# Kernel optimization log

Measured on AMD Instinct MI355X. Metric: run time of the kernel, lower is better.

Reference implementation:

```python
import jax, jax.numpy as jnp
import numpy as np

B = 64
A_DIM, T_DIM, V_DIM = 512, 1024, 512
H = 96
O1, O2, O3 = 6, 1, 3
HP1 = H + 1  # 97


def setup_inputs() -> dict:
    key = jax.random.key(0)
    ks = jax.random.split(key, 20)
    s = 0.02
    inp = {
        "audios": jax.random.normal(ks[0], (B, A_DIM), jnp.float32),
        "texts": jax.random.normal(ks[1], (B, T_DIM), jnp.float32),
        "videos": jax.random.normal(ks[2], (B, V_DIM), jnp.float32),
        # MLP encoders: Linear(in, hidden) + ReLU (dropout is identity at eval)
        "Wa": jax.random.normal(ks[3], (A_DIM, H), jnp.float32) * s,
        "ba": jnp.zeros((H,), jnp.float32),
        "Wt": jax.random.normal(ks[4], (T_DIM, H), jnp.float32) * s,
        "bt": jnp.zeros((H,), jnp.float32),
        "Wv": jax.random.normal(ks[5], (V_DIM, H), jnp.float32) * s,
        "bv": jnp.zeros((H,), jnp.float32),
        # post-fusion MLP
        "W1": jax.random.normal(ks[6], (HP1 * HP1 * HP1, H), jnp.float32) * s,
        "b1": jnp.zeros((H,), jnp.float32),
        "W2": jax.random.normal(ks[7], (H, H), jnp.float32) * s,
        "b2": jnp.zeros((H,), jnp.float32),
        # output heads
        "Wo1": jax.random.normal(ks[8], (H, O1), jnp.float32) * s,
        "bo1": jnp.zeros((O1,), jnp.float32),
        "Wo2": jax.random.normal(ks[9], (H, O2), jnp.float32) * s,
        "bo2": jnp.zeros((O2,), jnp.float32),
        "Wo3": jax.random.normal(ks[10], (H, O3), jnp.float32) * s,
        "bo3": jnp.zeros((O3,), jnp.float32),
    }
    return inp


def reference(audios, texts, videos, Wa, ba, Wt, bt, Wv, bv,
              W1, b1, W2, b2, Wo1, bo1, Wo2, bo2, Wo3, bo3):
    # encoders (eval mode: dropout = identity)
    ah = jax.nn.relu(audios @ Wa + ba)   # [B, H]
    th = jax.nn.relu(texts @ Wt + bt)    # [B, H]
    vh = jax.nn.relu(videos @ Wv + bv)   # [B, H]

    one = jnp.ones((ah.shape[0], 1), ah.dtype)
    a1 = jnp.concatenate([one, ah], axis=1)  # [B, H+1]
    v1 = jnp.concatenate([one, vh], axis=1)  # [B, H+1]
    t1 = jnp.concatenate([one, th], axis=1)  # [B, H+1]

    # trilinear outer product: bmm(a1[:, :, None], v1[:, None, :]) -> [B, A, V]
    # then bmm with t1 -> [B, A*V, T]; flatten order is (a, v, t)
    fusion = jnp.einsum('ba,bv,bt->bavt', a1, v1, t1).reshape(a1.shape[0], -1)

    y1 = jax.nn.relu(fusion @ W1 + b1)
    features = jax.nn.relu(y1 @ W2 + b2)

    emos_out = features @ Wo1 + bo1
    vals_out = features @ Wo2 + bo2
    sents_out = features @ Wo3 + bo3
    interloss = jnp.zeros((), jnp.float32)
    return (features, emos_out, vals_out, sents_out, interloss)
```

## Files before the change

kernel.cpp:

```cpp
#include <hip/hip_runtime.h>


typedef unsigned int u32;
typedef short frag8s __attribute__((ext_vector_type(8)));
typedef float f32x4 __attribute__((ext_vector_type(4)));

constexpr int G3     = 589;
constexpr int NRUN   = 9409;
constexpr int NRUNP  = 9412;
constexpr int NGROUP = 2353;
constexpr int RBLK   = 776;

constexpr int WS_A1T  = 0;
constexpr int WS_V1T  = WS_A1T + 98 * 64;
constexpr int WS_T1T  = WS_V1T + 98 * 64;
constexpr int WS_T1PK = WS_T1T + 98 * 64;
constexpr int WS_S    = WS_T1PK + 64 * 64;
constexpr int WS_WAT  = WS_S + NRUNP * 64;
constexpr int WS_WTT  = WS_WAT + 96 * 512;
constexpr int WS_WVT  = WS_WTT + 96 * 1024;
constexpr int WS_PART = WS_WVT + 96 * 512;
constexpr int WS_PART2= WS_PART + G3 * 6144;

__device__ __forceinline__ u32 bfrne(float x) {
    u32 u = __float_as_uint(x);
    return (u + 0x7FFFu + ((u >> 16) & 1u)) >> 16;
}
__device__ __forceinline__ float bflo(u32 p) { return __uint_as_float(p << 16); }
__device__ __forceinline__ float bfhi(u32 p) { return __uint_as_float(p & 0xFFFF0000u); }

__device__ __forceinline__ void async_cp16(float* lds, const float* g) {
    __builtin_amdgcn_global_load_lds((const __attribute__((address_space(1))) u32*)g,
                                     (__attribute__((address_space(3))) u32*)lds, 16, 0, 0);
}
__device__ __forceinline__ void async_cp4(float* lds, const float* g) {
    __builtin_amdgcn_global_load_lds((const __attribute__((address_space(1))) u32*)g,
                                     (__attribute__((address_space(3))) u32*)lds, 4, 0, 0);
}

__global__ void k0_transpose(const float* __restrict__ Wa, const float* __restrict__ Wt,
                             const float* __restrict__ Wv, float* __restrict__ ws) {
    int idx = blockIdx.x * 256 + threadIdx.x;
    if (idx < 49152) {
        int h = idx / 512, k = idx % 512;
        ws[WS_WAT + h * 512 + k] = Wa[k * 96 + h];
    } else if (idx < 147456) {
        int i = idx - 49152; int h = i / 1024, k = i % 1024;
        ws[WS_WTT + h * 1024 + k] = Wt[k * 96 + h];
    } else if (idx < 196608) {
        int i = idx - 147456; int h = i / 512, k = i % 512;
        ws[WS_WVT + h * 512 + k] = Wv[k * 96 + h];
    }
}

__global__ __launch_bounds__(256) void k1_enc(const float* __restrict__ audios,
                                              const float* __restrict__ texts,
                                              const float* __restrict__ videos,
                                              const float* __restrict__ ba,
                                              const float* __restrict__ bt,
                                              const float* __restrict__ bv,
                                              float* __restrict__ ws) {
    int wg = blockIdx.x, tid = threadIdx.x;
    int lane = tid & 63, wv = tid >> 6;
    if (wg == 288) {
        if (tid < 64) ws[WS_T1T + 97 * 64 + tid] = 0.0f;
        return;
    }
    int e = wg / 96, h = wg % 96;
    const float* in; const float* wt; float bias; int K; int outbase;
    if (e == 0)      { in = audios; wt = ws + WS_WAT + h * 512;  bias = ba[h]; K = 512;  outbase = WS_A1T; }
    else if (e == 1) { in = texts;  wt = ws + WS_WTT + h * 1024; bias = bt[h]; K = 1024; outbase = WS_T1T; }
    else             { in = videos; wt = ws + WS_WVT + h * 512;  bias = bv[h]; K = 512;  outbase = WS_V1T; }
    int nsweep = K >> 8;
    float4 wreg[4];
    for (int s = 0; s < nsweep; s++) wreg[s] = ((const float4*)wt)[s * 64 + lane];
    for (int pass = 0; pass < 16; pass++) {
        int b = pass * 4 + wv;
        float acc = 0.f;
        for (int s = 0; s < nsweep; s++) {
            float4 iv = ((const float4*)(in + b * K))[s * 64 + lane];
            acc += iv.x * wreg[s].x + iv.y * wreg[s].y + iv.z * wreg[s].z + iv.w * wreg[s].w;
        }
        for (int off = 32; off; off >>= 1) acc += __shfl_down(acc, off, 64);
        if (lane == 0) {
            float v = acc + bias;
            ws[outbase + (h + 1) * 64 + b] = v > 0.f ? v : 0.f;
        }
    }
    if (h == 0 && tid < 64) ws[outbase + tid] = 1.0f;
}

__global__ __launch_bounds__(256) void k2_s(float* __restrict__ ws) {
    int wg = blockIdx.x, tid = threadIdx.x;
    u32* t1pk = (u32*)ws + WS_T1PK;
    if (wg == 589) {
        for (int i = tid; i < 4096; i += 256) {
            int b = i >> 6, p = i & 63;
            u32 v = 0;
            if (p < 49) {
                float e0 = ws[WS_T1T + (2 * p) * 64 + b];
                float e1 = ws[WS_T1T + (2 * p + 1) * 64 + b];
                v = bfrne(e0) | (bfrne(e1) << 16);
            }
            t1pk[i] = v;
        }
        return;
    }
    for (int ii = 0; ii < 4; ii++) {
        int idx = wg * 1024 + ii * 256 + tid;
        if (idx >= NRUNP * 64) break;
        int run = idx >> 6, b = idx & 6 * 10 + 3;
        b = idx & 63;
        float s = 0.f;
        if (run < NRUN) {
            int i = run / 97, j = run % 97;
            s = ws[WS_A1T + i * 64 + b] * ws[WS_V1T + j * 64 + b];
        }
        ws[WS_S + idx] = s;
    }
}

__global__ __launch_bounds__(256) void k3_main(const float* __restrict__ W1,
                                               float* __restrict__ ws) {
    __shared__ float wtile[2][4 * RBLK];
    __shared__ u32   tpk[64 * 65];
    __shared__ float sl[2][4 * 64];

    int tid = threadIdx.x, lane = tid & 63, wv = tid >> 6;
    int id = blockIdx.x;
    const u32* t1pk_g = (const u32*)ws + WS_T1PK;
    const float* s_g = ws + WS_S;

    for (int i = tid; i < 2 * 4 * RBLK / 4; i += 256)
        ((float4*)wtile)[i] = make_float4(0.f, 0.f, 0.f, 0.f);
    for (int i = tid; i < 4096; i += 256) {
        int b = i >> 6, p = i & 63;
        tpk[b * 65 + p] = t1pk_g[i];
    }

    int glist[4]; int gcount = 0;
    for (int i2 = 0; i2 < 4; i2++) { int g = id + i2 * G3; if (g < NGROUP) glist[gcount++] = g; }

    f32x4 acc[6];
    for (int nt = 0; nt < 6; nt++) acc[nt] = f32x4{0.f, 0.f, 0.f, 0.f};

    auto stage_w = [&](int g, int koff, int buf) {
        int run = g * 4 + wv; if (run > 9408) run = 9408;
        if (koff < 96) {
            const float* gsrc = W1 + (size_t)(run * 97 + koff) * 96;
            float* ldst = &wtile[buf][wv * RBLK];
            for (int c = 0; c < 3; c++)
                async_cp16(ldst + c * 256, gsrc + c * 256 + lane * 4);
        } else {
            if (lane < 24)
                async_cp16(&wtile[buf][wv * RBLK], W1 + (size_t)(run * 97 + 96) * 96 + lane * 4);
        }
    };
    auto stage_s = [&](int g, int sb) {
        if (wv == 0) {
            for (int q2 = 0; q2 < 4; q2++) {
                int run = g * 4 + q2;
                async_cp4(&sl[sb][q2 * 64], s_g + run * 64 + lane);
            }
        }
    };

    stage_s(glist[0], 0);
    stage_w(glist[0], 0, 0);
    __syncthreads();

    int pw = 0, sb = 0;
    int b = (wv << 4) + (lane & 15);
    int q = lane >> 4;

    for (int gi = 0; gi < gcount; gi++) {
        int g = glist[gi];
        for (int step = 0; step < 13; step++) {
            int koff = step * 8;
            if (step < 12) stage_w(g, koff + 8, pw ^ 1);
            else if (gi + 1 < gcount) { stage_w(glist[gi + 1], 0, pw ^ 1); stage_s(glist[gi + 1], sb ^ 1); }

            float s = sl[sb][q * 64 + b];
            int pb = b * 65 + (koff >> 1);
            u32 ap[4];
#pragma unroll
            for (int r = 0; r < 4; r++) {
                u32 tp = tpk[pb + r];
                float fe = s * bflo(tp), fo = s * bfhi(tp);
                ap[r] = bfrne(fe) | (bfrne(fo) << 16);
            }
            union { u32 u[4]; frag8s f; } afr;
            afr.u[0] = ap[0]; afr.u[1] = ap[1]; afr.u[2] = ap[2]; afr.u[3] = ap[3];

            const float* wt0 = &wtile[pw][q * RBLK + (lane & 15)];
#pragma unroll
            for (int nt = 0; nt < 6; nt++) {
                union { u32 u[4]; frag8s f; } bfr;
#pragma unroll
                for (int r = 0; r < 4; r++) {
                    u32 w0 = __float_as_uint(wt0[(2 * r) * 96 + nt * 16]);
                    u32 w1 = __float_as_uint(wt0[(2 * r + 1) * 96 + nt * 16]);
                    bfr.u[r] = (w0 >> 16) | (w1 & 0xFFFF0000u);
                }
                acc[nt] = __builtin_amdgcn_mfma_f32_16x16x32_bf16(afr.f, bfr.f, acc[nt], 0, 0, 0);
            }
            __syncthreads();
            pw ^= 1;
        }
        sb ^= 1;
    }

    float* part = ws + WS_PART + (size_t)id * 6144;
#pragma unroll
    for (int nt = 0; nt < 6; nt++) {
#pragma unroll
        for (int r = 0; r < 4; r++) {
            int row = (wv << 4) + ((lane >> 4) << 2) + r;
            int col = nt * 16 + (lane & 15);
            part[row * 96 + col] = acc[nt][r];
        }
    }
}

__global__ __launch_bounds__(256) void k4a_reduce(float* __restrict__ ws) {
    int bid = blockIdx.x;
    int oc = bid % 24, wc = bid / 24;
    int o = oc * 256 + threadIdx.x;
    int w0 = wc * 74, w1 = w0 + 74; if (w1 > G3) w1 = G3;
    const float* part = ws + WS_PART + o;
    float a0 = 0.f, a1 = 0.f;
    int w = w0;
    for (; w + 2 <= w1; w += 2) {
        a0 += part[(size_t)w * 6144];
        a1 += part[(size_t)(w + 1) * 6144];
    }
    for (; w < w1; w++) a0 += part[(size_t)w * 6144];
    ws[WS_PART2 + (size_t)wc * 6144 + o] = a0 + a1;
}

__global__ __launch_bounds__(256) void k5_final(const float* __restrict__ b1,
                                                const float* __restrict__ W2, const float* __restrict__ b2,
                                                const float* __restrict__ Wo1, const float* __restrict__ bo1,
                                                const float* __restrict__ Wo2, const float* __restrict__ bo2,
                                                const float* __restrict__ Wo3, const float* __restrict__ bo3,
                                                const float* __restrict__ ws, float* __restrict__ out) {
    __shared__ float yl[8 * 96];
    __shared__ float w2l[96 * 97];
    __shared__ float fl[8 * 96];
    int tid = threadIdx.x;
    int row0 = blockIdx.x * 8;
    for (int i = tid; i < 768; i += 256) {
        int go = row0 * 96 + i;
        float acc = b1[i % 96];
#pragma unroll
        for (int w = 0; w < 8; w++) acc += ws[WS_PART2 + (size_t)w * 6144 + go];
        yl[i] = acc > 0.f ? acc : 0.f;
    }
    for (int i = tid; i < 9216; i += 256) { int k = i / 96, h = i % 96; w2l[k * 97 + h] = W2[i]; }
    __syncthreads();
    for (int i = tid; i < 768; i += 256) {
        int bb = i / 96, h = i % 96;
        float acc = b2[h];
#pragma unroll 8
        for (int k = 0; k < 96; k++) acc += yl[bb * 96 + k] * w2l[k * 97 + h];
        float f = acc > 0.f ? acc : 0.f;
        fl[i] = f; out[(row0 + bb) * 96 + h] = f;
    }
    __syncthreads();
    if (tid < 80) {
        if (tid < 48) {
            int lr = tid / 6, j = tid % 6;
            float acc = bo1[j];
            for (int k = 0; k < 96; k++) acc += fl[lr * 96 + k] * Wo1[k * 6 + j];
            out[6144 + (row0 + lr) * 6 + j] = acc;
        } else if (tid < 56) {
            int lr = tid - 48;
            float acc = bo2[0];
            for (int k = 0; k < 96; k++) acc += fl[lr * 96 + k] * Wo2[k];
            out[6528 + row0 + lr] = acc;
        } else {
            int t2 = tid - 56; int lr = t2 / 3, j = t2 % 3;
            float acc = bo3[j];
            for (int k = 0; k < 96; k++) acc += fl[lr * 96 + k] * Wo3[k * 3 + j];
            out[6592 + (row0 + lr) * 3 + j] = acc;
        }
    }
    if (blockIdx.x == 0 && tid == 0) out[6784] = 0.0f;
}

extern "C" void kernel_launch(void* const* d_in, const int* in_sizes, int n_in,
                              void* d_out, int out_size, void* d_ws, size_t ws_size,
                              hipStream_t stream) {
    (void)in_sizes; (void)n_in; (void)out_size; (void)ws_size;
    const float* audios = (const float*)d_in[0];
    const float* texts  = (const float*)d_in[1];
    const float* videos = (const float*)d_in[2];
    const float* Wa  = (const float*)d_in[3];
    const float* ba  = (const float*)d_in[4];
    const float* Wt  = (const float*)d_in[5];
    const float* bt  = (const float*)d_in[6];
    const float* Wv  = (const float*)d_in[7];
    const float* bv  = (const float*)d_in[8];
    const float* W1  = (const float*)d_in[9];
    const float* b1  = (const float*)d_in[10];
    const float* W2  = (const float*)d_in[11];
    const float* b2  = (const float*)d_in[12];
    const float* Wo1 = (const float*)d_in[13];
    const float* bo1 = (const float*)d_in[14];
    const float* Wo2 = (const float*)d_in[15];
    const float* bo2 = (const float*)d_in[16];
    const float* Wo3 = (const float*)d_in[17];
    const float* bo3 = (const float*)d_in[18];
    float* ws = (float*)d_ws;
    float* outp = (float*)d_out;

    k0_transpose<<<768, 256, 0, stream>>>(Wa, Wt, Wv, ws);
    k1_enc<<<289, 256, 0, stream>>>(audios, texts, videos, ba, bt, bv, ws);
    k2_s<<<590, 256, 0, stream>>>(ws);
    k3_main<<<G3, 256, 0, stream>>>(W1, ws);
    k4a_reduce<<<192, 256, 0, stream>>>(ws);
    k5_final<<<8, 256, 0, stream>>>(b1, W2, b2, Wo1, bo1, Wo2, bo2, Wo3, bo3, ws, outp);
}
```

Before: 583.8 us.

## Fuse prep kernels into main GEMM, deepen W1 pipeline, reduce via atomics

Result: faster. 565.5 us (-3.1%).

```diff
diff --git a/kernel.cpp b/kernel.cpp
--- a/kernel.cpp
+++ b/kernel.cpp
@@ -5,22 +5,16 @@
 typedef short frag8s __attribute__((ext_vector_type(8)));
 typedef float f32x4 __attribute__((ext_vector_type(4)));
 
-constexpr int G3     = 589;
 constexpr int NRUN   = 9409;
-constexpr int NRUNP  = 9412;
 constexpr int NGROUP = 2353;
 constexpr int RBLK   = 776;
-
-constexpr int WS_A1T  = 0;
-constexpr int WS_V1T  = WS_A1T + 98 * 64;
-constexpr int WS_T1T  = WS_V1T + 98 * 64;
-constexpr int WS_T1PK = WS_T1T + 98 * 64;
-constexpr int WS_S    = WS_T1PK + 64 * 64;
-constexpr int WS_WAT  = WS_S + NRUNP * 64;
-constexpr int WS_WTT  = WS_WAT + 96 * 512;
-constexpr int WS_WVT  = WS_WTT + 96 * 1024;
-constexpr int WS_PART = WS_WVT + 96 * 512;
-constexpr int WS_PART2= WS_PART + G3 * 6144;
+constexpr int NW1    = 912673 * 96;
+constexpr int G3     = 512;
+
+constexpr int WS_A1T   = 0;
+constexpr int WS_V1T   = WS_A1T + 98 * 64;
+constexpr int WS_T1T   = WS_V1T + 98 * 64;
+constexpr int WS_Y1SUM = WS_T1T + 98 * 64;
 
 __device__ __forceinline__ u32 bfrne(float x) {
     u32 u = __float_as_uint(x);
@@ -33,47 +27,33 @@
     __builtin_amdgcn_global_load_lds((const __attribute__((address_space(1))) u32*)g,
                                      (__attribute__((address_space(3))) u32*)lds, 16, 0, 0);
 }
-__device__ __forceinline__ void async_cp4(float* lds, const float* g) {
-    __builtin_amdgcn_global_load_lds((const __attribute__((address_space(1))) u32*)g,
-                                     (__attribute__((address_space(3))) u32*)lds, 4, 0, 0);
-}
-
-__global__ void k0_transpose(const float* __restrict__ Wa, const float* __restrict__ Wt,
-                             const float* __restrict__ Wv, float* __restrict__ ws) {
-    int idx = blockIdx.x * 256 + threadIdx.x;
-    if (idx < 49152) {
-        int h = idx / 512, k = idx % 512;
-        ws[WS_WAT + h * 512 + k] = Wa[k * 96 + h];
-    } else if (idx < 147456) {
-        int i = idx - 49152; int h = i / 1024, k = i % 1024;
-        ws[WS_WTT + h * 1024 + k] = Wt[k * 96 + h];
-    } else if (idx < 196608) {
-        int i = idx - 147456; int h = i / 512, k = i % 512;
-        ws[WS_WVT + h * 512 + k] = Wv[k * 96 + h];
-    }
-}
 
 __global__ __launch_bounds__(256) void k1_enc(const float* __restrict__ audios,
                                               const float* __restrict__ texts,
                                               const float* __restrict__ videos,
-                                              const float* __restrict__ ba,
-                                              const float* __restrict__ bt,
-                                              const float* __restrict__ bv,
+                                              const float* __restrict__ Wa, const float* __restrict__ ba,
+                                              const float* __restrict__ Wt, const float* __restrict__ bt,
+                                              const float* __restrict__ Wv, const float* __restrict__ bv,
                                               float* __restrict__ ws) {
     int wg = blockIdx.x, tid = threadIdx.x;
     int lane = tid & 63, wv = tid >> 6;
     if (wg == 288) {
         if (tid < 64) ws[WS_T1T + 97 * 64 + tid] = 0.0f;
+        for (int i = tid; i < 6144; i += 256) ws[WS_Y1SUM + i] = 0.0f;
         return;
     }
     int e = wg / 96, h = wg % 96;
-    const float* in; const float* wt; float bias; int K; int outbase;
-    if (e == 0)      { in = audios; wt = ws + WS_WAT + h * 512;  bias = ba[h]; K = 512;  outbase = WS_A1T; }
-    else if (e == 1) { in = texts;  wt = ws + WS_WTT + h * 1024; bias = bt[h]; K = 1024; outbase = WS_T1T; }
-    else             { in = videos; wt = ws + WS_WVT + h * 512;  bias = bv[h]; K = 512;  outbase = WS_V1T; }
+    const float* in; const float* W; float bias; int K; int outbase;
+    if (e == 0)      { in = audios; W = Wa; bias = ba[h]; K = 512;  outbase = WS_A1T; }
+    else if (e == 1) { in = texts;  W = Wt; bias = bt[h]; K = 1024; outbase = WS_T1T; }
+    else             { in = videos; W = Wv; bias = bv[h]; K = 512;  outbase = WS_V1T; }
     int nsweep = K >> 8;
     float4 wreg[4];
-    for (int s = 0; s < nsweep; s++) wreg[s] = ((const float4*)wt)[s * 64 + lane];
+    for (int s = 0; s < nsweep; s++) {
+        int k0i = s * 256 + lane * 4;
+        wreg[s] = make_float4(W[(k0i + 0) * 96 + h], W[(k0i + 1) * 96 + h],
+                              W[(k0i + 2) * 96 + h], W[(k0i + 3) * 96 + h]);
+    }
     for (int pass = 0; pass < 16; pass++) {
         int b = pass * 4 + wv;
         float acc = 0.f;
@@ -90,152 +70,117 @@
     if (h == 0 && tid < 64) ws[outbase + tid] = 1.0f;
 }
 
-__global__ __launch_bounds__(256) void k2_s(float* __restrict__ ws) {
-    int wg = blockIdx.x, tid = threadIdx.x;
-    u32* t1pk = (u32*)ws + WS_T1PK;
-    if (wg == 589) {
-        for (int i = tid; i < 4096; i += 256) {
-            int b = i >> 6, p = i & 63;
-            u32 v = 0;
-            if (p < 49) {
-                float e0 = ws[WS_T1T + (2 * p) * 64 + b];
-                float e1 = ws[WS_T1T + (2 * p + 1) * 64 + b];
-                v = bfrne(e0) | (bfrne(e1) << 16);
-            }
-            t1pk[i] = v;
-        }
-        return;
-    }
-    for (int ii = 0; ii < 4; ii++) {
-        int idx = wg * 1024 + ii * 256 + tid;
-        if (idx >= NRUNP * 64) break;
-        int run = idx >> 6, b = idx & 6 * 10 + 3;
-        b = idx & 63;
-        float s = 0.f;
-        if (run < NRUN) {
-            int i = run / 97, j = run % 97;
-            s = ws[WS_A1T + i * 64 + b] * ws[WS_V1T + j * 64 + b];
-        }
-        ws[WS_S + idx] = s;
-    }
-}
-
 __global__ __launch_bounds__(256) void k3_main(const float* __restrict__ W1,
                                                float* __restrict__ ws) {
-    __shared__ float wtile[2][4 * RBLK];
+    __shared__ float wtile[4][4 * RBLK];
     __shared__ u32   tpk[64 * 65];
-    __shared__ float sl[2][4 * 64];
+    __shared__ float sl[5][256];
 
     int tid = threadIdx.x, lane = tid & 63, wv = tid >> 6;
     int id = blockIdx.x;
-    const u32* t1pk_g = (const u32*)ws + WS_T1PK;
-    const float* s_g = ws + WS_S;
-
-    for (int i = tid; i < 2 * 4 * RBLK / 4; i += 256)
-        ((float4*)wtile)[i] = make_float4(0.f, 0.f, 0.f, 0.f);
+    int g0, gcount;
+    if (id < 305) { g0 = id * 5;                 gcount = 5; }
+    else          { g0 = 1525 + (id - 305) * 4;  gcount = 4; }
+    const int L = gcount * 13;
+
     for (int i = tid; i < 4096; i += 256) {
-        int b = i >> 6, p = i & 63;
-        tpk[b * 65 + p] = t1pk_g[i];
-    }
-
-    int glist[4]; int gcount = 0;
-    for (int i2 = 0; i2 < 4; i2++) { int g = id + i2 * G3; if (g < NGROUP) glist[gcount++] = g; }
+        int b_ = i >> 6, p = i & 63;
+        u32 v = 0;
+        if (p < 49) {
+            float e0 = ws[WS_T1T + (2 * p) * 64 + b_];
+            float e1 = ws[WS_T1T + (2 * p + 1) * 64 + b_];
+            v = bfrne(e0) | (bfrne(e1) << 16);
+        }
+        tpk[b_ * 65 + p] = v;
+    }
+    {
+        int q2 = tid >> 6, b_ = tid & 63;
+#pragma unroll
+        for (int g2 = 0; g2 < 5; g2++) {
+            float s = 0.f;
+            int run = (g0 + g2) * 4 + q2;
+            if (g2 < gcount && run < NRUN) {
+                int i = run / 97, j = run % 97;
+                s = ws[WS_A1T + i * 64 + b_] * ws[WS_V1T + j * 64 + b_];
+            }
+            sl[g2][tid] = s;
+        }
+    }
+
+    auto stage = [&](int g, int t, int buf) {
+        int idx0 = (g * 4 + wv) * (97 * 96) + t * (8 * 96) + lane * 4;
+        float* ldst = &wtile[buf][wv * RBLK];
+#pragma unroll
+        for (int c = 0; c < 3; c++) {
+            int idx = idx0 + c * 256;
+            idx = idx < NW1 - 4 ? idx : NW1 - 4;
+            async_cp16(ldst + c * 256, W1 + idx);
+        }
+    };
+    int cs_g = g0, cs_t = 0;
+    auto stage_next = [&](int buf) {
+        stage(cs_g, cs_t, buf);
+        if (++cs_t == 13) { cs_t = 0; ++cs_g; }
+    };
+
+    stage_next(0); stage_next(1); stage_next(2);
+    asm volatile("s_waitcnt vmcnt(6) lgkmcnt(0)" ::: "memory");
+    __builtin_amdgcn_s_barrier();
 
     f32x4 acc[6];
+#pragma unroll
     for (int nt = 0; nt < 6; nt++) acc[nt] = f32x4{0.f, 0.f, 0.f, 0.f};
 
-    auto stage_w = [&](int g, int koff, int buf) {
-        int run = g * 4 + wv; if (run > 9408) run = 9408;
-        if (koff < 96) {
-            const float* gsrc = W1 + (size_t)(run * 97 + koff) * 96;
-            float* ldst = &wtile[buf][wv * RBLK];
-            for (int c = 0; c < 3; c++)
-                async_cp16(ldst + c * 256, gsrc + c * 256 + lane * 4);
-        } else {
-            if (lane < 24)
-                async_cp16(&wtile[buf][wv * RBLK], W1 + (size_t)(run * 97 + 96) * 96 + lane * 4);
-        }
-    };
-    auto stage_s = [&](int g, int sb) {
-        if (wv == 0) {
-            for (int q2 = 0; q2 < 4; q2++) {
-                int run = g * 4 + q2;
-                async_cp4(&sl[sb][q2 * 64], s_g + run * 64 + lane);
-            }
-        }
-    };
-
-    stage_s(glist[0], 0);
-    stage_w(glist[0], 0, 0);
-    __syncthreads();
-
-    int pw = 0, sb = 0;
     int b = (wv << 4) + (lane & 15);
     int q = lane >> 4;
 
-    for (int gi = 0; gi < gcount; gi++) {
-        int g = glist[gi];
-        for (int step = 0; step < 13; step++) {
-            int koff = step * 8;
-            if (step < 12) stage_w(g, koff + 8, pw ^ 1);
-            else if (gi + 1 < gcount) { stage_w(glist[gi + 1], 0, pw ^ 1); stage_s(glist[gi + 1], sb ^ 1); }
-
-            float s = sl[sb][q * 64 + b];
-            int pb = b * 65 + (koff >> 1);
-            u32 ap[4];
+    int gi = 0, t = 0;
+    for (int u = 0; u < L; ++u) {
+        if (u + 3 < L) stage_next((u + 3) & 3);
+
+        float sv = sl[gi][q * 64 + b];
+        int pb = b * 65 + t * 4;
+        u32 ap[4];
+#pragma unroll
+        for (int r = 0; r < 4; r++) {
+            u32 tp = tpk[pb + r];
+            float fe = sv * bflo(tp), fo = sv * bfhi(tp);
+            ap[r] = bfrne(fe) | (bfrne(fo) << 16);
+        }
+        union { u32 u4[4]; frag8s f; } afr;
+        afr.u4[0] = ap[0]; afr.u4[1] = ap[1]; afr.u4[2] = ap[2]; afr.u4[3] = ap[3];
+
+        const float* wt0 = &wtile[u & 3][q * RBLK + (lane & 15)];
+#pragma unroll
+        for (int nt = 0; nt < 6; nt++) {
+            union { u32 u4[4]; frag8s f; } bfr;
 #pragma unroll
             for (int r = 0; r < 4; r++) {
-                u32 tp = tpk[pb + r];
-                float fe = s * bflo(tp), fo = s * bfhi(tp);
-                ap[r] = bfrne(fe) | (bfrne(fo) << 16);
+                u32 w0 = __float_as_uint(wt0[(2 * r) * 96 + nt * 16]);
+                u32 w1 = __float_as_uint(wt0[(2 * r + 1) * 96 + nt * 16]);
+                bfr.u4[r] = (w0 >> 16) | (w1 & 0xFFFF0000u);
             }
-            union { u32 u[4]; frag8s f; } afr;
-            afr.u[0] = ap[0]; afr.u[1] = ap[1]; afr.u[2] = ap[2]; afr.u[3] = ap[3];
-
-            const float* wt0 = &wtile[pw][q * RBLK + (lane & 15)];
-#pragma unroll
-            for (int nt = 0; nt < 6; nt++) {
-                union { u32 u[4]; frag8s f; } bfr;
-#pragma unroll
-                for (int r = 0; r < 4; r++) {
-                    u32 w0 = __float_as_uint(wt0[(2 * r) * 96 + nt * 16]);
-                    u32 w1 = __float_as_uint(wt0[(2 * r + 1) * 96 + nt * 16]);
-                    bfr.u[r] = (w0 >> 16) | (w1 & 0xFFFF0000u);
-                }
-                acc[nt] = __builtin_amdgcn_mfma_f32_16x16x32_bf16(afr.f, bfr.f, acc[nt], 0, 0, 0);
-            }
-            __syncthreads();
-            pw ^= 1;
-        }
-        sb ^= 1;
-    }
-
-    float* part = ws + WS_PART + (size_t)id * 6144;
+            acc[nt] = __builtin_amdgcn_mfma_f32_16x16x32_bf16(afr.f, bfr.f, acc[nt], 0, 0, 0);
+        }
+
+        if (u + 4 <= L)      asm volatile("s_waitcnt vmcnt(6) lgkmcnt(0)" ::: "memory");
+        else if (u + 3 == L) asm volatile("s_waitcnt vmcnt(3) lgkmcnt(0)" ::: "memory");
+        else                 asm volatile("s_waitcnt vmcnt(0) lgkmcnt(0)" ::: "memory");
+        __builtin_amdgcn_s_barrier();
+
+        if (++t == 13) { t = 0; ++gi; }
+    }
+
+    float* ysum = ws + WS_Y1SUM;
 #pragma unroll
     for (int nt = 0; nt < 6; nt++) {
 #pragma unroll
         for (int r = 0; r < 4; r++) {
             int row = (wv << 4) + ((lane >> 4) << 2) + r;
             int col = nt * 16 + (lane & 15);
-            part[row * 96 + col] = acc[nt][r];
-        }
-    }
-}
-
-__global__ __launch_bounds__(256) void k4a_reduce(float* __restrict__ ws) {
-    int bid = blockIdx.x;
-    int oc = bid % 24, wc = bid / 24;
-    int o = oc * 256 + threadIdx.x;
-    int w0 = wc * 74, w1 = w0 + 74; if (w1 > G3) w1 = G3;
-    const float* part = ws + WS_PART + o;
-    float a0 = 0.f, a1 = 0.f;
-    int w = w0;
-    for (; w + 2 <= w1; w += 2) {
-        a0 += part[(size_t)w * 6144];
-        a1 += part[(size_t)(w + 1) * 6144];
-    }
-    for (; w < w1; w++) a0 += part[(size_t)w * 6144];
-    ws[WS_PART2 + (size_t)wc * 6144 + o] = a0 + a1;
+            atomicAdd(&ysum[row * 96 + col], acc[nt][r]);
+        }
+    }
 }
 
 __global__ __launch_bounds__(256) void k5_final(const float* __restrict__ b1,
@@ -251,9 +196,7 @@
     int row0 = blockIdx.x * 8;
     for (int i = tid; i < 768; i += 256) {
         int go = row0 * 96 + i;
-        float acc = b1[i % 96];
-#pragma unroll
-        for (int w = 0; w < 8; w++) acc += ws[WS_PART2 + (size_t)w * 6144 + go];
+        float acc = b1[i % 96] + ws[WS_Y1SUM + go];
         yl[i] = acc > 0.f ? acc : 0.f;
     }
     for (int i = tid; i < 9216; i += 256) { int k = i / 96, h = i % 96; w2l[k * 97 + h] = W2[i]; }
@@ -314,10 +257,7 @@
     float* ws = (float*)d_ws;
     float* outp = (float*)d_out;
 
-    k0_transpose<<<768, 256, 0, stream>>>(Wa, Wt, Wv, ws);
-    k1_enc<<<289, 256, 0, stream>>>(audios, texts, videos, ba, bt, bv, ws);
-    k2_s<<<590, 256, 0, stream>>>(ws);
+    k1_enc<<<289, 256, 0, stream>>>(audios, texts, videos, Wa, ba, Wt, bt, Wv, bv, ws);
     k3_main<<<G3, 256, 0, stream>>>(W1, ws);
-    k4a_reduce<<<192, 256, 0, stream>>>(ws);
     k5_final<<<8, 256, 0, stream>>>(b1, W2, b2, Wo1, bo1, Wo2, bo2, Wo3, bo3, ws, outp);
 }
```
